# Optimization experiments

Hardware: AMD Instinct MI355X
Metric: run time of the kernel (lower is better)

## Reference

```python
import jax, jax.numpy as jnp
import numpy as np
from jax import lax

M = 32        # matrixSize
NMAX = 9      # color_code_number


def _conv3(x, w, b):
    # 3x3, stride 1, pad 1 (spatial-preserving), NCHW/OIHW
    y = lax.conv_general_dilated(x, w, (1, 1), ((1, 1), (1, 1)),
                                 dimension_numbers=('NCHW', 'OIHW', 'NCHW'))
    return y + b[None, :, None, None]


def _cnn(x, masks, w1, b1, w2, b2, w3, b3, fcw, fcb):
    # x: [1, C, H, W]; masks: [NM, H, W] int (binary regions)
    c = x.shape[1]
    xv = x.reshape(c, -1)                       # [C, H*W]
    feat = xv
    n = min(NMAX, masks.shape[0])
    # per-mask mean subtraction; later masks overwrite (index_copy_ semantics),
    # mean always taken from the ORIGINAL features x_view
    for i in range(n):
        m = (masks[i].reshape(-1) > 0).astype(x.dtype)
        cnt = m.sum()
        valid = cnt >= 10.0
        mean = (xv * m).sum(axis=1, keepdims=True) / jnp.maximum(cnt, 1.0)
        feat = jnp.where((m > 0) & valid, xv - mean, feat)
    f = _conv3(jax.nn.relu(_conv3(jax.nn.relu(_conv3(feat.reshape(x.shape), w1, b1)), w2, b2)), w3, b3)
    fv = f.reshape(f.shape[1], -1)              # [M, H*W]
    mats, valids = [], []
    for i in range(n):
        m = (masks[i].reshape(-1) == 1).astype(x.dtype)
        cnt = m.sum()
        sel = fv * m                            # masked gather as multiply
        cov = (sel @ sel.T) / jnp.maximum(cnt, 1.0)   # [M, M]
        mats.append(fcw @ cov.reshape(-1) + fcb)      # fc on flattened cov
        valids.append(cnt >= 10.0)
    return jnp.stack(mats), jnp.stack(valids), feat


def _forward(cF, sF, cmasks, smasks, sp, cp, compress_w, compress_b, unzip_w, unzip_b):
    sMats, svalid, _ = _cnn(sF, smasks, *sp)
    cMats, cvalid, cF_sub = _cnn(cF, cmasks, *cp)
    ccv = compress_w @ cF_sub + compress_b[:, None]   # 1x1 conv -> [M, H*W]
    trans = ccv
    sFF = sF.reshape(sF.shape[1], -1)                 # [C, H*W]
    finalSMean = jnp.zeros((cF.shape[1], cF.shape[2] * cF.shape[3]), cF.dtype)
    n = min(NMAX, cmasks.shape[0], smasks.shape[0])
    for i in range(n):
        cm = (cmasks[i].reshape(-1) == 1).astype(cF.dtype)
        sm = (smasks[i].reshape(-1) == 1).astype(cF.dtype)
        valid = (cm.sum() >= 10.0) & (sm.sum() >= 10.0) & svalid[i] & cvalid[i]
        sMean = (sFF * sm).sum(axis=1, keepdims=True) / jnp.maximum(sm.sum(), 1.0)
        tm = sMats[i].reshape(M, M) @ cMats[i].reshape(M, M)
        trans = jnp.where((cm > 0) & valid, tm @ ccv, trans)
        finalSMean = jnp.where((cm > 0) & valid, sMean, finalSMean)
    out = (unzip_w @ trans + unzip_b[:, None]).reshape(cF.shape)  # 1x1 unzip
    return out + finalSMean.reshape(cF.shape)


def setup_inputs() -> dict:
    key = jax.random.key(0)
    ks = jax.random.split(key, 32)
    H = W = 256
    C = 512
    NM = 4

    def p(k, shape, s=0.05):
        return jax.random.normal(k, shape, jnp.float32) * s

    inp = {
        'cF': jax.random.normal(ks[0], (1, C, H, W), jnp.float32),
        'sF': jax.random.normal(ks[1], (1, C, H, W), jnp.float32),
        'cmasks': jax.random.randint(ks[2], (NM, H, W), 0, 2, jnp.int32),
        'smasks': jax.random.randint(ks[3], (NM, H, W), 0, 2, jnp.int32),
        # snet CNN (r41): 512->256->128->32, fc 1024->1024
        'snet_w1': p(ks[4], (256, 512, 3, 3)), 'snet_b1': jnp.zeros(256, jnp.float32),
        'snet_w2': p(ks[5], (128, 256, 3, 3)), 'snet_b2': jnp.zeros(128, jnp.float32),
        'snet_w3': p(ks[6], (M, 128, 3, 3)), 'snet_b3': jnp.zeros(M, jnp.float32),
        'snet_fcw': p(ks[7], (M * M, M * M)), 'snet_fcb': jnp.zeros(M * M, jnp.float32),
        # cnet CNN
        'cnet_w1': p(ks[8], (256, 512, 3, 3)), 'cnet_b1': jnp.zeros(256, jnp.float32),
        'cnet_w2': p(ks[9], (128, 256, 3, 3)), 'cnet_b2': jnp.zeros(128, jnp.float32),
        'cnet_w3': p(ks[10], (M, 128, 3, 3)), 'cnet_b3': jnp.zeros(M, jnp.float32),
        'cnet_fcw': p(ks[11], (M * M, M * M)), 'cnet_fcb': jnp.zeros(M * M, jnp.float32),
        # compress / unzip 1x1 convs as [O, I] matmuls
        'compress_w': p(ks[12], (M, C)), 'compress_b': jnp.zeros(M, jnp.float32),
        'unzip_w': p(ks[13], (C, M)), 'unzip_b': jnp.zeros(C, jnp.float32),
    }
    return inp


def reference(cF, sF, cmasks, smasks,
              snet_w1, snet_b1, snet_w2, snet_b2, snet_w3, snet_b3, snet_fcw, snet_fcb,
              cnet_w1, cnet_b1, cnet_w2, cnet_b2, cnet_w3, cnet_b3, cnet_fcw, cnet_fcb,
              compress_w, compress_b, unzip_w, unzip_b):
    sp = (snet_w1, snet_b1, snet_w2, snet_b2, snet_w3, snet_b3, snet_fcw, snet_fcb)
    cp = (cnet_w1, cnet_b1, cnet_w2, cnet_b2, cnet_w3, cnet_b3, cnet_fcw, cnet_fcb)
    return _forward(cF, sF, cmasks, smasks, sp, cp, compress_w, compress_b, unzip_w, unzip_b)
```

## Files before the change

kernel.cpp:

```cpp
#include <hip/hip_runtime.h>

#define HDIM 256
#define WDIM 256
#define HW   65536
#define CDIM 512

using bf16x8 = __attribute__((ext_vector_type(8))) short;
using f32x4  = __attribute__((ext_vector_type(4))) float;

__device__ __forceinline__ unsigned short f2bf(float f) {
    unsigned u = __builtin_bit_cast(unsigned, f);
    u += 0x7FFFu + ((u >> 16) & 1u);
    return (unsigned short)(u >> 16);
}

__device__ __forceinline__ void gload_lds16(const void* g, void* l) {
    __builtin_amdgcn_global_load_lds((const __attribute__((address_space(1))) unsigned int*)g,
                                     (__attribute__((address_space(3))) unsigned int*)l, 16, 0, 0);
}


__global__ __launch_bounds__(256) void zero_small_k(int* __restrict__ cnt,
                                                    float* __restrict__ covraw,
                                                    float* __restrict__ zp) {
    int t = blockIdx.x * 256 + threadIdx.x;
    if (t < 8) cnt[t] = 0;
    if (t < 8192) covraw[t] = 0.f;
    if (t < 64) zp[t] = 0.f;
}

__global__ __launch_bounds__(256) void pack_masks_k(const int* __restrict__ cm,
                                                    const int* __restrict__ sm,
                                                    int n,
                                                    unsigned char* __restrict__ ccode,
                                                    unsigned char* __restrict__ scode,
                                                    int* __restrict__ cnt) {
    int p = blockIdx.x * 256 + threadIdx.x;
    unsigned cc = 0, sc = 0;
    for (int i = 0; i < n; ++i) {
        if (cm[i * HW + p] != 0) cc |= (1u << i);
        if (sm[i * HW + p] != 0) sc |= (1u << i);
    }
    ccode[p] = (unsigned char)cc;
    scode[p] = (unsigned char)sc;
    int lane = threadIdx.x & 63;
    for (int i = 0; i < n; ++i) {
        unsigned long long bc = __ballot((cc >> i) & 1);
        unsigned long long bs = __ballot((sc >> i) & 1);
        if (lane == 0) {
            atomicAdd(&cnt[i],     (int)__popcll(bc));
            atomicAdd(&cnt[4 + i], (int)__popcll(bs));
        }
    }
}

__global__ __launch_bounds__(256) void masked_means_k(const float* __restrict__ cF,
                                                      const float* __restrict__ sF,
                                                      const unsigned char* __restrict__ ccode,
                                                      const unsigned char* __restrict__ scode,
                                                      const int* __restrict__ cnt,
                                                      float* __restrict__ cmean5,
                                                      float* __restrict__ smean5) {
    int b = blockIdx.x;
    const float* x; const unsigned char* code; const int* cn; float* mout;
    if (b < CDIM) { x = cF; code = ccode; cn = cnt;     mout = cmean5; }
    else          { x = sF; code = scode; cn = cnt + 4; mout = smean5; b -= CDIM; }
    const int c = b;
    const int t = threadIdx.x;
    const float4* x4 = (const float4*)(x + (size_t)c * HW);
    const unsigned* cd4 = (const unsigned*)code;
    float s0 = 0.f, s1 = 0.f, s2 = 0.f, s3 = 0.f;
    for (int i = t; i < HW / 4; i += 256) {
        float4 v = x4[i];
        unsigned cd = cd4[i];
        float vv;
        vv = v.x;
        if (cd & 0x01u) s0 += vv;
        if (cd & 0x02u) s1 += vv;
        if (cd & 0x04u) s2 += vv;
        if (cd & 0x08u) s3 += vv;
        vv = v.y;
        if (cd & 0x0100u) s0 += vv;
        if (cd & 0x0200u) s1 += vv;
        if (cd & 0x0400u) s2 += vv;
        if (cd & 0x0800u) s3 += vv;
        vv = v.z;
        if (cd & 0x010000u) s0 += vv;
        if (cd & 0x020000u) s1 += vv;
        if (cd & 0x040000u) s2 += vv;
        if (cd & 0x080000u) s3 += vv;
        vv = v.w;
        if (cd & 0x01000000u) s0 += vv;
        if (cd & 0x02000000u) s1 += vv;
        if (cd & 0x04000000u) s2 += vv;
        if (cd & 0x08000000u) s3 += vv;
    }
    __shared__ float red[4][256];
    red[0][t] = s0; red[1][t] = s1; red[2][t] = s2; red[3][t] = s3;
    __syncthreads();
    for (int off = 128; off; off >>= 1) {
        if (t < off) {
            red[0][t] += red[0][t + off];
            red[1][t] += red[1][t + off];
            red[2][t] += red[2][t + off];
            red[3][t] += red[3][t + off];
        }
        __syncthreads();
    }
    if (t < 4) mout[t * CDIM + c] = red[t][0] / fmaxf((float)cn[t], 1.f);
    if (t == 4) mout[4 * CDIM + c] = 0.f;
}

__global__ __launch_bounds__(256) void idx_maps_k(const unsigned char* __restrict__ ccode,
                                                  const unsigned char* __restrict__ scode,
                                                  const int* __restrict__ cnt, int n,
                                                  signed char* __restrict__ cidx,
                                                  signed char* __restrict__ sidx,
                                                  signed char* __restrict__ fidx) {
    int p = blockIdx.x * 256 + threadIdx.x;
    int cc = ccode[p], sc = scode[p];
    int ci = 4, si = 4, fi = 4;
    for (int i = 0; i < n; ++i) {
        bool cv = cnt[i] >= 10;
        bool sv = cnt[4 + i] >= 10;
        if (((cc >> i) & 1) && cv) ci = i;
        if (((sc >> i) & 1) && sv) si = i;
        if (((cc >> i) & 1) && cv && sv) fi = i;
    }
    cidx[p] = (signed char)ci;
    sidx[p] = (signed char)si;
    fidx[p] = (signed char)fi;
}


__global__ __launch_bounds__(256) void wtrans_k(const float* __restrict__ w,
                                                unsigned short* __restrict__ wt,
                                                int COUT, int CIN) {
    int t = blockIdx.x * 256 + threadIdx.x;
    int total = COUT * CIN * 9;
    if (t >= total) return;
    int oc = t / (CIN * 9);
    int rem = t - oc * (CIN * 9);
    int ci = rem / 9;
    int tap = rem - ci * 9;
    wt[(size_t)(((ci >> 5) * 9 + tap) * COUT + oc) * 32 + (ci & 31)] = f2bf(w[t]);
}

__global__ __launch_bounds__(256) void wctrans_k(const float* __restrict__ w,
                                                 unsigned short* __restrict__ wc) {
    int t = blockIdx.x * 256 + threadIdx.x;
    if (t >= 32 * 512) return;
    int oc = t >> 9, ci = t & 511;
    wc[(size_t)((ci >> 5) * 32 + oc) * 32 + (ci & 31)] = f2bf(w[t]);
}

__global__ __launch_bounds__(256) void trans_in_k(const float* __restrict__ X,
                                                  const float* __restrict__ mean5,
                                                  const signed char* __restrict__ idx5,
                                                  unsigned short* __restrict__ Xt) {
    __shared__ unsigned s32[64 * 33];
    const int tid = threadIdx.x;
    const int p0 = blockIdx.x * 64;
    const int c0 = blockIdx.y * 64;
    const int cpair = tid >> 3;
    const int q = tid & 7;
    const int ch0 = c0 + cpair * 2;
    const float* X0 = X + (size_t)ch0 * HW;
    const float* X1 = X0 + HW;
#pragma unroll
    for (int k = 0; k < 2; ++k) {
        int px0 = (q + k * 8) * 4;
        float4 va = *(const float4*)(X0 + p0 + px0);
        float4 vb = *(const float4*)(X1 + p0 + px0);
        int id4 = *(const int*)(idx5 + p0 + px0);
        float a[4] = {va.x, va.y, va.z, va.w};
        float b[4] = {vb.x, vb.y, vb.z, vb.w};
#pragma unroll
        for (int j = 0; j < 4; ++j) {
            int id = (id4 >> (8 * j)) & 0xFF;
            const float* mr = mean5 + id * CDIM;
            unsigned u = (unsigned)f2bf(a[j] - mr[ch0])
                       | ((unsigned)f2bf(b[j] - mr[ch0 + 1]) << 16);
            s32[(px0 + j) * 33 + cpair] = u;
        }
    }
    __syncthreads();
    const int px = tid >> 2, h = tid & 3;
    const unsigned* rp = &s32[px * 33 + h * 8];
    uint4 u0 = *(const uint4*)(rp);
    uint4 u1 = *(const uint4*)(rp + 4);
    unsigned short* dst = Xt + (size_t)(p0 + px) * CDIM + c0 + h * 16;
    *(uint4*)dst = u0;
    *(uint4*)(dst + 8) = u1;
}

template <int CIN, int COUT, int BM, int BN, bool RELU>
__global__ __launch_bounds__(256, 2) void convmf2_k(const unsigned short* __restrict__ Xt,
                                                    const unsigned short* __restrict__ Wt,
                                                    const float* __restrict__ bias,
                                                    unsigned short* __restrict__ Yt,
                                                    const unsigned short* __restrict__ zp) {
    constexpr int WM = BM / 4;
    constexpr int FM = WM / 16;
    constexpr int FN = BN / 16;
    constexpr int PXT = BN + 2;
    constexpr int PXTP = BN + 6;
    constexpr int NCH = 12 * PXTP;
    constexpr int NCHP = (NCH + 255) & ~255;
    constexpr int NCB = CIN / 32;
    __shared__ unsigned short s_tile[2][NCHP * 8];

    const int tid = threadIdx.x;
    const int ln = tid & 63, wid = tid >> 6;
    const int ln15 = ln & 15, g = ln >> 4;

    constexpr int TPR = WDIM / BN;
    const int y0 = blockIdx.x / TPR;
    const int x0 = (blockIdx.x % TPR) * BN;
    const int ocb = blockIdx.y * BM;

    auto stage = [&](int buf, int cb) {
#pragma unroll
        for (int c0 = 0; c0 < NCH; c0 += 256) {
            int c = c0 + tid;
            if (c < NCH) {
                int grow = c / PXTP;
                int px = c - grow * PXTP;
                int ky = grow >> 2, gg = grow & 3;
                int y = y0 + ky - 1;
                int x = x0 - 1 + px;
                bool ok = (px < PXT) && ((unsigned)y < HDIM) && ((unsigned)x < WDIM);
                const unsigned short* src = ok
                    ? Xt + (size_t)(y * WDIM + x) * CIN + cb * 32 + gg * 8
                    : zp;
                gload_lds16(src, &s_tile[buf][(size_t)(c0 + wid * 64) * 8]);
            }
        }
    };

    f32x4 acc[FM][FN];
#pragma unroll
    for (int i = 0; i < FM; ++i)
#pragma unroll
        for (int j = 0; j < FN; ++j) acc[i][j] = f32x4{0.f, 0.f, 0.f, 0.f};

    const unsigned short* wfb = Wt + (size_t)(ocb + wid * WM + ln15) * 32 + g * 8;

    stage(0, 0);

    for (int cb = 0; cb < NCB; ++cb) {
        const int buf = cb & 1;
        __syncthreads();
        bf16x8 wreg[9][FM];
#pragma unroll
        for (int tap = 0; tap < 9; ++tap)
#pragma unroll
            for (int mf = 0; mf < FM; ++mf)
                wreg[tap][mf] = *(const bf16x8*)(wfb + (size_t)((cb * 9 + tap) * COUT + mf * 16) * 32);
        if (cb + 1 < NCB) stage(buf ^ 1, cb + 1);
        const unsigned short* st = &s_tile[buf][0];
#pragma unroll
        for (int tap = 0; tap < 9; ++tap) {
            const int ky = tap / 3, kx = tap - ky * 3;
            bf16x8 b[FN];
#pragma unroll
            for (int nf = 0; nf < FN; ++nf) {
                int slot = (ky * 4 + g) * PXTP + kx + nf * 16 + ln15;
                b[nf] = *(const bf16x8*)&st[(size_t)slot * 8];
            }
#pragma unroll
            for (int mf = 0; mf < FM; ++mf)
#pragma unroll
                for (int nf = 0; nf < FN; ++nf)
                    acc[mf][nf] = __builtin_amdgcn_mfma_f32_16x16x32_bf16(wreg[tap][mf], b[nf], acc[mf][nf], 0, 0, 0);
        }
    }

    const int p0 = y0 * WDIM + x0;
#pragma unroll
    for (int nf = 0; nf < FN; ++nf) {
        const size_t p = (size_t)p0 + nf * 16 + ln15;
#pragma unroll
        for (int mf = 0; mf < FM; ++mf) {
            const int oc0 = ocb + wid * WM + mf * 16 + g * 4;
            const float4 bi = *(const float4*)(bias + oc0);
            f32x4 v = acc[mf][nf];
            float r0 = v[0] + bi.x, r1 = v[1] + bi.y, r2 = v[2] + bi.z, r3 = v[3] + bi.w;
            if (RELU) {
                r0 = fmaxf(r0, 0.f); r1 = fmaxf(r1, 0.f);
                r2 = fmaxf(r2, 0.f); r3 = fmaxf(r3, 0.f);
            }
            unsigned lo = (unsigned)f2bf(r0) | ((unsigned)f2bf(r1) << 16);
            unsigned hi = (unsigned)f2bf(r2) | ((unsigned)f2bf(r3) << 16);
            *(uint2*)(Yt + p * COUT + oc0) = uint2{lo, hi};
        }
    }
}

template <int CIN, int COUT, int BM, int BN, int WM, int WN, bool RELU>
__global__ __launch_bounds__(256, 2) void convmf_k(const unsigned short* __restrict__ Xt,
                                                   const unsigned short* __restrict__ Wt,
                                                   const float* __restrict__ bias,
                                                   float* __restrict__ Yf,
                                                   const unsigned short* __restrict__ zp) {
    constexpr int WAVES_N = BN / WN;
    constexpr int FM = WM / 16, FN = WN / 16;
    constexpr int PXT = BN + 2;
    constexpr int PXTP = BN + 6;
    constexpr int NCH = 12 * PXTP;
    constexpr int NCHP = (NCH + 255) & ~255;
    __shared__ unsigned short s_tile[NCHP * 8];

    const int tid = threadIdx.x;
    const int ln = tid & 63, wid = tid >> 6;
    const int ln15 = ln & 15, g = ln >> 4;
    const int wm_i = wid / WAVES_N, wn_i = wid % WAVES_N;

    constexpr int TPR = WDIM / BN;
    const int y0 = blockIdx.x / TPR;
    const int x0 = (blockIdx.x % TPR) * BN;
    const int ocb = blockIdx.y * BM;

    f32x4 acc[FM][FN];
#pragma unroll
    for (int i = 0; i < FM; ++i)
#pragma unroll
        for (int j = 0; j < FN; ++j) acc[i][j] = f32x4{0.f, 0.f, 0.f, 0.f};

    const unsigned short* wfb = Wt + (size_t)(ocb + wm_i * WM + ln15) * 32 + g * 8;

    for (int cb = 0; cb < CIN / 32; ++cb) {
        __syncthreads();
        for (int c0 = 0; c0 < NCH; c0 += 256) {
            int c = c0 + tid;
            if (c < NCH) {
                int grow = c / PXTP;
                int px = c - grow * PXTP;
                int ky = grow >> 2, gg = grow & 3;
                int y = y0 + ky - 1;
                int x = x0 - 1 + px;
                bool ok = (px < PXT) && ((unsigned)y < HDIM) && ((unsigned)x < WDIM);
                const unsigned short* src = ok
                    ? Xt + (size_t)(y * WDIM + x) * CIN + cb * 32 + gg * 8
                    : zp;
                gload_lds16(src, &s_tile[(size_t)(c0 + wid * 64) * 8]);
            }
        }
        bf16x8 wreg[9][FM];
#pragma unroll
        for (int tap = 0; tap < 9; ++tap)
#pragma unroll
            for (int mf = 0; mf < FM; ++mf)
                wreg[tap][mf] = *(const bf16x8*)(wfb + (size_t)((cb * 9 + tap) * COUT + mf * 16) * 32);
        __syncthreads();
#pragma unroll
        for (int tap = 0; tap < 9; ++tap) {
            const int ky = tap / 3, kx = tap - ky * 3;
            bf16x8 b[FN];
#pragma unroll
            for (int nf = 0; nf < FN; ++nf) {
                int slot = (ky * 4 + g) * PXTP + kx + wn_i * WN + nf * 16 + ln15;
                b[nf] = *(const bf16x8*)&s_tile[(size_t)slot * 8];
            }
#pragma unroll
            for (int mf = 0; mf < FM; ++mf)
#pragma unroll
                for (int nf = 0; nf < FN; ++nf)
                    acc[mf][nf] = __builtin_amdgcn_mfma_f32_16x16x32_bf16(wreg[tap][mf], b[nf], acc[mf][nf], 0, 0, 0);
        }
    }

    const int p0 = y0 * WDIM + x0;
#pragma unroll
    for (int nf = 0; nf < FN; ++nf) {
        const size_t p = (size_t)p0 + wn_i * WN + nf * 16 + ln15;
#pragma unroll
        for (int mf = 0; mf < FM; ++mf) {
            const int oc0 = ocb + wm_i * WM + mf * 16 + g * 4;
            const float4 bi = *(const float4*)(bias + oc0);
            f32x4 v = acc[mf][nf];
            float r0 = v[0] + bi.x, r1 = v[1] + bi.y, r2 = v[2] + bi.z, r3 = v[3] + bi.w;
            if (RELU) {
                r0 = fmaxf(r0, 0.f); r1 = fmaxf(r1, 0.f);
                r2 = fmaxf(r2, 0.f); r3 = fmaxf(r3, 0.f);
            }
            Yf[(size_t)(oc0 + 0) * HW + p] = r0;
            Yf[(size_t)(oc0 + 1) * HW + p] = r1;
            Yf[(size_t)(oc0 + 2) * HW + p] = r2;
            Yf[(size_t)(oc0 + 3) * HW + p] = r3;
        }
    }
}

__global__ __launch_bounds__(256, 2) void ccv_gemm_k(const unsigned short* __restrict__ Xt,
                                                     const unsigned short* __restrict__ wc,
                                                     const float* __restrict__ cbias,
                                                     float* __restrict__ ccv) {
    __shared__ unsigned short s_t[1024 * 8];
    const int tid = threadIdx.x;
    const int ln = tid & 63, wid = tid >> 6;
    const int ln15 = ln & 15, g = ln >> 4;
    const int p0 = blockIdx.x * 256;

    f32x4 acc[2][4];
#pragma unroll
    for (int i = 0; i < 2; ++i)
#pragma unroll
        for (int j = 0; j < 4; ++j) acc[i][j] = f32x4{0.f, 0.f, 0.f, 0.f};

    for (int cb = 0; cb < 16; ++cb) {
        __syncthreads();
#pragma unroll
        for (int pass = 0; pass < 4; ++pass) {
            int c = pass * 256 + tid;
            int gg = c >> 8, px = c & 255;
            const unsigned short* src = Xt + (size_t)(p0 + px) * CDIM + cb * 32 + gg * 8;
            gload_lds16(src, &s_t[(size_t)c * 8]);
        }
        bf16x8 a[2];
#pragma unroll
        for (int mf = 0; mf < 2; ++mf)
            a[mf] = *(const bf16x8*)(wc + (size_t)((cb * 32 + mf * 16 + ln15) * 32) + g * 8);
        __syncthreads();
        bf16x8 b[4];
#pragma unroll
        for (int nf = 0; nf < 4; ++nf) {
            int slot = g * 256 + wid * 64 + nf * 16 + ln15;
            b[nf] = *(const bf16x8*)&s_t[(size_t)slot * 8];
        }
#pragma unroll
        for (int mf = 0; mf < 2; ++mf)
#pragma unroll
            for (int nf = 0; nf < 4; ++nf)
                acc[mf][nf] = __builtin_amdgcn_mfma_f32_16x16x32_bf16(a[mf], b[nf], acc[mf][nf], 0, 0, 0);
    }
#pragma unroll
    for (int nf = 0; nf < 4; ++nf) {
        const size_t p = (size_t)p0 + wid * 64 + nf * 16 + ln15;
#pragma unroll
        for (int mf = 0; mf < 2; ++mf) {
            const int oc0 = mf * 16 + g * 4;
            const float4 bi = *(const float4*)(cbias + oc0);
            f32x4 v = acc[mf][nf];
            ccv[(size_t)(oc0 + 0) * HW + p] = v[0] + bi.x;
            ccv[(size_t)(oc0 + 1) * HW + p] = v[1] + bi.y;
            ccv[(size_t)(oc0 + 2) * HW + p] = v[2] + bi.z;
            ccv[(size_t)(oc0 + 3) * HW + p] = v[3] + bi.w;
        }
    }
}


__global__ __launch_bounds__(256) void cov_accum_k(const float* __restrict__ f,
                                                   const unsigned char* __restrict__ code,
                                                   float* __restrict__ covraw) {
    constexpr int PCH = 256;
    __shared__ float s_f[32][PCH + 1];
    const int i = blockIdx.y;
    const int p0 = blockIdx.x * PCH;
    const int t = threadIdx.x;
    for (int e = t; e < 32 * PCH; e += 256) {
        int row = e >> 8, col = e & (PCH - 1);
        int p = p0 + col;
        float m = ((code[p] >> i) & 1u) ? 1.f : 0.f;
        s_f[row][col] = f[(size_t)row * HW + p] * m;
    }
    __syncthreads();
    const int a = t >> 3;
    const int b0 = (t & 7) * 4;
    float a0 = 0.f, a1 = 0.f, a2 = 0.f, a3 = 0.f;
    for (int p = 0; p < PCH; ++p) {
        float va = s_f[a][p];
        a0 = fmaf(va, s_f[b0 + 0][p], a0);
        a1 = fmaf(va, s_f[b0 + 1][p], a1);
        a2 = fmaf(va, s_f[b0 + 2][p], a2);
        a3 = fmaf(va, s_f[b0 + 3][p], a3);
    }
    float* dst = covraw + i * 1024 + a * 32 + b0;
    atomicAdd(dst + 0, a0);
    atomicAdd(dst + 1, a1);
    atomicAdd(dst + 2, a2);
    atomicAdd(dst + 3, a3);
}

__global__ __launch_bounds__(256) void fc_k(const float* __restrict__ fcw,
                                            const float* __restrict__ fcb,
                                            const float* __restrict__ covraw,
                                            const int* __restrict__ cnt,
                                            float* __restrict__ mats) {
    const int i = blockIdx.y;
    const int wv = threadIdx.x >> 6;
    const int lane = threadIdx.x & 63;
    const int r = blockIdx.x * 4 + wv;
    const float inv = 1.f / fmaxf((float)cnt[i], 1.f);
    float acc = 0.f;
    for (int q = lane; q < 1024; q += 64)
        acc = fmaf(fcw[r * 1024 + q], covraw[i * 1024 + q] * inv, acc);
    for (int off = 32; off; off >>= 1) acc += __shfl_down(acc, off);
    if (lane == 0) mats[i * 1024 + r] = acc + fcb[r];
}

__global__ __launch_bounds__(256) void prep_small_k(const float* __restrict__ sMats,
                                                    const float* __restrict__ cMats,
                                                    const float* __restrict__ unzip_b,
                                                    const float* __restrict__ smean5,
                                                    int n,
                                                    float* __restrict__ tm5,
                                                    float* __restrict__ B5) {
    int t = blockIdx.x * 256 + threadIdx.x;
    if (t < 5 * 1024) {
        int i = t >> 10, rc = t & 1023, r = rc >> 5, c = rc & 31;
        float v;
        if (i < n) {
            float s = 0.f;
            for (int k = 0; k < 32; ++k)
                s = fmaf(sMats[i * 1024 + r * 32 + k], cMats[i * 1024 + k * 32 + c], s);
            v = s;
        } else {
            v = (r == c) ? 1.f : 0.f;
        }
        tm5[t] = v;
    } else if (t < 5 * 1024 + 5 * 512) {
        int u = t - 5 * 1024;
        int i = u >> 9, c = u & 511;
        B5[u] = unzip_b[c] + smean5[i * CDIM + c];
    }
}

__global__ __launch_bounds__(256) void final_k(const float* __restrict__ ccv,
                                               const signed char* __restrict__ fidx,
                                               const float* __restrict__ tm5,
                                               const float* __restrict__ B5,
                                               const float* __restrict__ uw,
                                               float* __restrict__ out) {
    __shared__ float s_tm[5 * 1032];
    __shared__ float s_B[5 * 520];
    const int t = threadIdx.x;
    for (int e = t; e < 5 * 1024; e += 256) {
        int i = e >> 10, rc = e & 1023;
        s_tm[i * 1032 + rc] = tm5[e];
    }
    for (int e = t; e < 5 * 512; e += 256) {
        int i = e >> 9, c = e & 511;
        s_B[i * 520 + c] = B5[e];
    }
    __syncthreads();
    const int p = blockIdx.x * 256 + t;
    const int id = fidx[p];
    float v[32];
#pragma unroll
    for (int k = 0; k < 32; ++k) v[k] = ccv[(size_t)k * HW + p];
    float tv[32];
#pragma unroll
    for (int r = 0; r < 32; ++r) {
        float s = 0.f;
#pragma unroll
        for (int k = 0; k < 32; ++k)
            s = fmaf(s_tm[id * 1032 + r * 32 + k], v[k], s);
        tv[r] = s;
    }
    for (int c = 0; c < CDIM; ++c) {
        float s = s_B[id * 520 + c];
#pragma unroll
        for (int k = 0; k < 32; ++k)
            s = fmaf(uw[c * 32 + k], tv[k], s);
        out[(size_t)c * HW + p] = s;
    }
}


extern "C" void kernel_launch(void* const* d_in, const int* in_sizes, int n_in,
                              void* d_out, int out_size, void* d_ws, size_t ws_size,
                              hipStream_t stream) {
    const float* cF = (const float*)d_in[0];
    const float* sF = (const float*)d_in[1];
    const int* cmasks = (const int*)d_in[2];
    const int* smasks = (const int*)d_in[3];
    const float* snet_w1 = (const float*)d_in[4];
    const float* snet_b1 = (const float*)d_in[5];
    const float* snet_w2 = (const float*)d_in[6];
    const float* snet_b2 = (const float*)d_in[7];
    const float* snet_w3 = (const float*)d_in[8];
    const float* snet_b3 = (const float*)d_in[9];
    const float* snet_fcw = (const float*)d_in[10];
    const float* snet_fcb = (const float*)d_in[11];
    const float* cnet_w1 = (const float*)d_in[12];
    const float* cnet_b1 = (const float*)d_in[13];
    const float* cnet_w2 = (const float*)d_in[14];
    const float* cnet_b2 = (const float*)d_in[15];
    const float* cnet_w3 = (const float*)d_in[16];
    const float* cnet_b3 = (const float*)d_in[17];
    const float* cnet_fcw = (const float*)d_in[18];
    const float* cnet_fcb = (const float*)d_in[19];
    const float* compress_w = (const float*)d_in[20];
    const float* compress_b = (const float*)d_in[21];
    const float* unzip_w = (const float*)d_in[22];
    const float* unzip_b = (const float*)d_in[23];
    float* out = (float*)d_out;

    int nmC = in_sizes[2] / HW;
    int nmS = in_sizes[3] / HW;
    int n = nmC < nmS ? nmC : nmS;
    if (n > 4) n = 4;

    char* ws = (char*)d_ws;
    size_t off = 0;
    auto alloc = [&](size_t bytes) {
        size_t o = off;
        off += (bytes + 255) & ~(size_t)255;
        return o;
    };
    char* regA = ws + alloc((size_t)HW * 512 * 2);
    char* regB = ws + alloc((size_t)HW * 256 * 2);
    float* ccv  = (float*)(ws + alloc((size_t)32 * HW * 4));
    unsigned short* Wt1 = (unsigned short*)(ws + alloc((size_t)9 * 256 * 512 * 2));
    unsigned short* Wt2 = (unsigned short*)(ws + alloc((size_t)9 * 128 * 256 * 2));
    unsigned short* Wt3 = (unsigned short*)(ws + alloc((size_t)9 * 32 * 128 * 2));
    unsigned short* Wc  = (unsigned short*)(ws + alloc((size_t)32 * 512 * 2));
    unsigned char* ccode = (unsigned char*)(ws + alloc(HW));
    unsigned char* scode = (unsigned char*)(ws + alloc(HW));
    signed char* cidx = (signed char*)(ws + alloc(HW));
    signed char* sidx = (signed char*)(ws + alloc(HW));
    signed char* fidx = (signed char*)(ws + alloc(HW));
    int*   cnt    = (int*)(ws + alloc(8 * 4));
    float* cmean5 = (float*)(ws + alloc(5 * CDIM * 4));
    float* smean5 = (float*)(ws + alloc(5 * CDIM * 4));
    float* covraw = (float*)(ws + alloc(8 * 1024 * 4));
    float* sMats  = (float*)(ws + alloc(4 * 1024 * 4));
    float* cMats  = (float*)(ws + alloc(4 * 1024 * 4));
    float* tm5    = (float*)(ws + alloc(5 * 1024 * 4));
    float* B5     = (float*)(ws + alloc(5 * 512 * 4));
    float* zpf    = (float*)(ws + alloc(256));
    (void)ws_size; (void)n_in; (void)out_size;

    unsigned short* Xt = (unsigned short*)regA;
    unsigned short* Y2 = (unsigned short*)regA;
    unsigned short* Y1 = (unsigned short*)regB;
    float*          fbuf = (float*)regB;
    const unsigned short* zp = (const unsigned short*)zpf;

    zero_small_k<<<32, 256, 0, stream>>>(cnt, covraw, zpf);
    pack_masks_k<<<HW / 256, 256, 0, stream>>>(cmasks, smasks, n, ccode, scode, cnt);
    masked_means_k<<<2 * CDIM, 256, 0, stream>>>(cF, sF, ccode, scode, cnt, cmean5, smean5);
    idx_maps_k<<<HW / 256, 256, 0, stream>>>(ccode, scode, cnt, n, cidx, sidx, fidx);
    wctrans_k<<<(32 * 512 + 255) / 256, 256, 0, stream>>>(compress_w, Wc);

    wtrans_k<<<(9 * 256 * 512 + 255) / 256, 256, 0, stream>>>(snet_w1, Wt1, 256, 512);
    wtrans_k<<<(9 * 128 * 256 + 255) / 256, 256, 0, stream>>>(snet_w2, Wt2, 128, 256);
    wtrans_k<<<(9 * 32 * 128 + 255) / 256, 256, 0, stream>>>(snet_w3, Wt3, 32, 128);
    trans_in_k<<<dim3(HW / 64, 8), 256, 0, stream>>>(sF, smean5, sidx, Xt);
    convmf2_k<512, 256, 128, 128, true ><<<dim3(512, 2), 256, 0, stream>>>(Xt, Wt1, snet_b1, Y1, zp);
    convmf2_k<256, 128, 128, 128, true ><<<dim3(512, 1), 256, 0, stream>>>(Y1, Wt2, snet_b2, Y2, zp);
    convmf_k<128, 32,  32,  256, 32, 64, false><<<dim3(256, 1), 256, 0, stream>>>(Y2, Wt3, snet_b3, fbuf, zp);
    cov_accum_k<<<dim3(HW / 256, n), 256, 0, stream>>>(fbuf, scode, covraw);
    fc_k<<<dim3(256, n), 256, 0, stream>>>(snet_fcw, snet_fcb, covraw, cnt + 4, sMats);

    wtrans_k<<<(9 * 256 * 512 + 255) / 256, 256, 0, stream>>>(cnet_w1, Wt1, 256, 512);
    wtrans_k<<<(9 * 128 * 256 + 255) / 256, 256, 0, stream>>>(cnet_w2, Wt2, 128, 256);
    wtrans_k<<<(9 * 32 * 128 + 255) / 256, 256, 0, stream>>>(cnet_w3, Wt3, 32, 128);
    trans_in_k<<<dim3(HW / 64, 8), 256, 0, stream>>>(cF, cmean5, cidx, Xt);
    ccv_gemm_k<<<HW / 256, 256, 0, stream>>>(Xt, Wc, compress_b, ccv);
    convmf2_k<512, 256, 128, 128, true ><<<dim3(512, 2), 256, 0, stream>>>(Xt, Wt1, cnet_b1, Y1, zp);
    convmf2_k<256, 128, 128, 128, true ><<<dim3(512, 1), 256, 0, stream>>>(Y1, Wt2, cnet_b2, Y2, zp);
    convmf_k<128, 32,  32,  256, 32, 64, false><<<dim3(256, 1), 256, 0, stream>>>(Y2, Wt3, cnet_b3, fbuf, zp);
    cov_accum_k<<<dim3(HW / 256, n), 256, 0, stream>>>(fbuf, ccode, covraw + 4 * 1024);
    fc_k<<<dim3(256, n), 256, 0, stream>>>(cnet_fcw, cnet_fcb, covraw + 4 * 1024, cnt, cMats);

    prep_small_k<<<30, 256, 0, stream>>>(sMats, cMats, unzip_b, smean5, n, tm5, B5);
    final_k<<<HW / 256, 256, 0, stream>>>(ccv, fidx, tm5, B5, unzip_w, out);
}
```

Baseline: 1.043 ms.

## Cover all output channels per block in conv1/conv2 with 512-thread 4x2 wave grid

Replaces the 256-thread conv kernel with a 512-thread variant. Its eight waves are arranged 4 (output channels) by 2 (pixels), and each block computes every output channel for a 128-pixel row segment. The input halo tile is now staged into LDS once per pixel tile, instead of once per output-channel block. This removes the duplicated input traffic in the first conv, which previously split into two channel blocks. The cost is heavier register pressure for the 256-channel conv, where each wave holds 4x4 accumulators plus 36 weight fragments. Under a 2-blocks-per-CU launch bound this could cause spills or lower occupancy.

Measured after the change: 1.194 ms. 1.15x slower.

```diff
diff --git a/kernel.cpp b/kernel.cpp
--- a/kernel.cpp
+++ b/kernel.cpp
@@ -194,34 +194,33 @@
     *(uint4*)(dst + 8) = u1;
 }
 
-template <int CIN, int COUT, int BM, int BN, bool RELU>
-__global__ __launch_bounds__(256, 2) void convmf2_k(const unsigned short* __restrict__ Xt,
+template <int CIN, int COUT, bool RELU>
+__global__ __launch_bounds__(512, 2) void convmf3_k(const unsigned short* __restrict__ Xt,
                                                     const unsigned short* __restrict__ Wt,
                                                     const float* __restrict__ bias,
                                                     unsigned short* __restrict__ Yt,
                                                     const unsigned short* __restrict__ zp) {
-    constexpr int WM = BM / 4;
+    constexpr int BN = 128;
+    constexpr int WM = COUT / 4;
     constexpr int FM = WM / 16;
-    constexpr int FN = BN / 16;
+    constexpr int FN = 4;
     constexpr int PXT = BN + 2;
     constexpr int PXTP = BN + 6;
     constexpr int NCH = 12 * PXTP;
-    constexpr int NCHP = (NCH + 255) & ~255;
     constexpr int NCB = CIN / 32;
-    __shared__ unsigned short s_tile[2][NCHP * 8];
+    __shared__ unsigned short s_tile[2][NCH * 8];
 
     const int tid = threadIdx.x;
     const int ln = tid & 63, wid = tid >> 6;
     const int ln15 = ln & 15, g = ln >> 4;
-
-    constexpr int TPR = WDIM / BN;
-    const int y0 = blockIdx.x / TPR;
-    const int x0 = (blockIdx.x % TPR) * BN;
-    const int ocb = blockIdx.y * BM;
+    const int wm_i = wid >> 1, wn_i = wid & 1;
+
+    const int y0 = blockIdx.x >> 1;
+    const int x0 = (blockIdx.x & 1) * BN;
 
     auto stage = [&](int buf, int cb) {
 #pragma unroll
-        for (int c0 = 0; c0 < NCH; c0 += 256) {
+        for (int c0 = 0; c0 < NCH; c0 += 512) {
             int c = c0 + tid;
             if (c < NCH) {
                 int grow = c / PXTP;
@@ -244,7 +243,7 @@
 #pragma unroll
         for (int j = 0; j < FN; ++j) acc[i][j] = f32x4{0.f, 0.f, 0.f, 0.f};
 
-    const unsigned short* wfb = Wt + (size_t)(ocb + wid * WM + ln15) * 32 + g * 8;
+    const unsigned short* wfb = Wt + (size_t)(wm_i * WM + ln15) * 32 + g * 8;
 
     stage(0, 0);
 
@@ -265,7 +264,7 @@
             bf16x8 b[FN];
 #pragma unroll
             for (int nf = 0; nf < FN; ++nf) {
-                int slot = (ky * 4 + g) * PXTP + kx + nf * 16 + ln15;
+                int slot = (ky * 4 + g) * PXTP + kx + wn_i * 64 + nf * 16 + ln15;
                 b[nf] = *(const bf16x8*)&st[(size_t)slot * 8];
             }
 #pragma unroll
@@ -279,10 +278,10 @@
     const int p0 = y0 * WDIM + x0;
 #pragma unroll
     for (int nf = 0; nf < FN; ++nf) {
-        const size_t p = (size_t)p0 + nf * 16 + ln15;
+        const size_t p = (size_t)p0 + wn_i * 64 + nf * 16 + ln15;
 #pragma unroll
         for (int mf = 0; mf < FM; ++mf) {
-            const int oc0 = ocb + wid * WM + mf * 16 + g * 4;
+            const int oc0 = wm_i * WM + mf * 16 + g * 4;
             const float4 bi = *(const float4*)(bias + oc0);
             f32x4 v = acc[mf][nf];
             float r0 = v[0] + bi.x, r1 = v[1] + bi.y, r2 = v[2] + bi.z, r3 = v[3] + bi.w;
@@ -649,8 +648,8 @@
     wtrans_k<<<(9 * 128 * 256 + 255) / 256, 256, 0, stream>>>(snet_w2, Wt2, 128, 256);
     wtrans_k<<<(9 * 32 * 128 + 255) / 256, 256, 0, stream>>>(snet_w3, Wt3, 32, 128);
     trans_in_k<<<dim3(HW / 64, 8), 256, 0, stream>>>(sF, smean5, sidx, Xt);
-    convmf2_k<512, 256, 128, 128, true ><<<dim3(512, 2), 256, 0, stream>>>(Xt, Wt1, snet_b1, Y1, zp);
-    convmf2_k<256, 128, 128, 128, true ><<<dim3(512, 1), 256, 0, stream>>>(Y1, Wt2, snet_b2, Y2, zp);
+    convmf3_k<512, 256, true><<<512, 512, 0, stream>>>(Xt, Wt1, snet_b1, Y1, zp);
+    convmf3_k<256, 128, true><<<512, 512, 0, stream>>>(Y1, Wt2, snet_b2, Y2, zp);
     convmf_k<128, 32,  32,  256, 32, 64, false><<<dim3(256, 1), 256, 0, stream>>>(Y2, Wt3, snet_b3, fbuf, zp);
     cov_accum_k<<<dim3(HW / 256, n), 256, 0, stream>>>(fbuf, scode, covraw);
     fc_k<<<dim3(256, n), 256, 0, stream>>>(snet_fcw, snet_fcb, covraw, cnt + 4, sMats);
@@ -660,8 +659,8 @@
     wtrans_k<<<(9 * 32 * 128 + 255) / 256, 256, 0, stream>>>(cnet_w3, Wt3, 32, 128);
     trans_in_k<<<dim3(HW / 64, 8), 256, 0, stream>>>(cF, cmean5, cidx, Xt);
     ccv_gemm_k<<<HW / 256, 256, 0, stream>>>(Xt, Wc, compress_b, ccv);
-    convmf2_k<512, 256, 128, 128, true ><<<dim3(512, 2), 256, 0, stream>>>(Xt, Wt1, cnet_b1, Y1, zp);
-    convmf2_k<256, 128, 128, 128, true ><<<dim3(512, 1), 256, 0, stream>>>(Y1, Wt2, cnet_b2, Y2, zp);
+    convmf3_k<512, 256, true><<<512, 512, 0, stream>>>(Xt, Wt1, cnet_b1, Y1, zp);
+    convmf3_k<256, 128, true><<<512, 512, 0, stream>>>(Y1, Wt2, cnet_b2, Y2, zp);
     convmf_k<128, 32,  32,  256, 32, 64, false><<<dim3(256, 1), 256, 0, stream>>>(Y2, Wt3, cnet_b3, fbuf, zp);
     cov_accum_k<<<dim3(HW / 256, n), 256, 0, stream>>>(fbuf, ccode, covraw + 4 * 1024);
     fc_k<<<dim3(256, n), 256, 0, stream>>>(cnet_fcw, cnet_fcb, covraw + 4 * 1024, cnt, cMats);
```
